# Performance work log

Hardware: AMD Instinct MI355X
Metric: run time of the kernel (lower is better)

Reference implementation:

```python
import jax, jax.numpy as jnp
import numpy as np

HID = 512      # hidden_dim
SEQ = 784      # sequence length hard-coded via make_discrete_HiPPO_nojit(hidden, 784)
BATCH = 1024
OUT = 10


def make_discrete_hippo(N, L):
    # HiPPO-LegS continuous matrices (standard construction)
    n = np.arange(N, dtype=np.float64)
    P = np.sqrt(1.0 + 2.0 * n)
    A = P[:, None] * P[None, :]
    A = -(np.tril(A) - np.diag(n))          # (N, N)
    B = np.sqrt(2.0 * n + 1.0).reshape(N, 1)  # (N, 1)
    # bilinear (Tustin) discretization with step = 1/L
    step = 1.0 / L
    I = np.eye(N)
    BL = np.linalg.inv(I - (step / 2.0) * A)
    Ad = BL @ (I + (step / 2.0) * A)
    Bd = (BL * step) @ B
    return jnp.asarray(Ad, jnp.float32), jnp.asarray(Bd[:, 0], jnp.float32)


def setup_inputs() -> dict:
    key = jax.random.key(0)
    k1, k2, k3, k4 = jax.random.split(key, 4)
    x = jax.random.normal(k1, (BATCH, SEQ), jnp.float32)
    # xavier-uniform C params (flax nn.initializers.xavier_uniform)
    a0 = float(np.sqrt(6.0 / (1 + HID)))
    a1 = float(np.sqrt(6.0 / (HID + HID)))
    C0 = jax.random.uniform(k2, (1, HID), jnp.float32, -a0, a0)
    C1 = jax.random.uniform(k3, (HID, HID), jnp.float32, -a1, a1)
    # final Dense(output_dim): lecun_normal kernel, zero bias
    W = jax.random.normal(k4, (HID, OUT), jnp.float32) / np.sqrt(HID)
    b = jnp.zeros((OUT,), jnp.float32)
    return {"x": x, "C0": C0, "C1": C1, "W": W, "b": b}


def _ssm_layer(A, Bvec, C, u):
    # u: (batch, seq) scalar input per step; returns ys: (seq, batch, d_out)
    def step(h, u_t):  # h: (batch, HID), u_t: (batch,)
        h_next = jnp.tanh(h @ A.T + u_t[:, None] * Bvec[None, :])
        y = h_next @ C.T
        return h_next, y
    h0 = jnp.zeros((u.shape[0], HID), u.dtype)
    _, ys = jax.lax.scan(step, h0, u.T)
    return ys


def reference(x, C0, C1, W, b):
    A, Bvec = make_discrete_hippo(HID, SEQ)  # trace-time constants
    y0 = _ssm_layer(A, Bvec, C0, x)[:, :, 0].T   # (batch, seq) scalar stream
    y1 = _ssm_layer(A, Bvec, C1, y0)             # (seq, batch, HID)
    logits = y1[-1] @ W + b                      # last timestep -> Dense
    return logits
```

## Files before the change

kernel.cpp:

```cpp
#include <hip/hip_runtime.h>
#include <math.h>

#define SEQL 784
#define HIDN 512
#define OUTD 10

typedef float v2 __attribute__((ext_vector_type(2)));

template<int CTRL, int RM>
__device__ __forceinline__ float dpp0(float v) {
    int r = __builtin_amdgcn_update_dpp(0, __builtin_bit_cast(int, v),
                                        CTRL, RM, 0xF, true);
    return __builtin_bit_cast(float, r);
}
__device__ __forceinline__ v2 sp(float v) { v2 r; r.x = v; r.y = v; return r; }
__device__ __forceinline__ v2 vfma(v2 a, v2 b, v2 c) {
    return __builtin_elementwise_fma(a, b, c);
}

__global__ __launch_bounds__(256) void compute_M(const float* __restrict__ C1,
                                                 const float* __restrict__ W,
                                                 float* __restrict__ M) {
    __shared__ float Ws[HIDN * OUTD];
    __shared__ float red[4][64][OUTD];
    const int lane = threadIdx.x & 63, w = threadIdx.x >> 6;
    const int i = blockIdx.x * 64 + lane;
    for (int idx = threadIdx.x; idx < HIDN * OUTD; idx += 256) Ws[idx] = W[idx];
    __syncthreads();
    float acc[OUTD];
#pragma unroll
    for (int o = 0; o < OUTD; ++o) acc[o] = 0.f;
    for (int j = w * 128; j < w * 128 + 128; ++j) {
        float cv = C1[j * HIDN + i];
#pragma unroll
        for (int o = 0; o < OUTD; ++o) acc[o] = fmaf(cv, Ws[j * OUTD + o], acc[o]);
    }
#pragma unroll
    for (int o = 0; o < OUTD; ++o) red[w][lane][o] = acc[o];
    __syncthreads();
    if (w == 0) {
#pragma unroll
        for (int o = 0; o < OUTD; ++o)
            M[i * OUTD + o] = (red[0][lane][o] + red[1][lane][o]) +
                              (red[2][lane][o] + red[3][lane][o]);
    }
}

#define LVL(CTRL, RM, L) {                                                   \
        s.x = fmaf(dpp0<CTRL, RM>(s.x), bc[L], s.x);                         \
        s.x = fmaf(dpp0<CTRL, RM>(r.x), ac[L], s.x);                         \
        s.y = fmaf(dpp0<CTRL, RM>(s.y), bc[L], s.y);                         \
        s.y = fmaf(dpp0<CTRL, RM>(r.y), ac[L], s.y);                         \
        r.x += dpp0<CTRL, RM>(r.x);                                          \
        r.y += dpp0<CTRL, RM>(r.y); }

template<int PSEL>
static __device__ __forceinline__ float do_step(
        v2 (&H)[8], v2 du,
        const float (&P2)[8], const float (&G2)[8], const float (&mE2)[8],
        const float (&K_)[8], const float (&Psp)[8],
        const float (&C0d2)[8], float PiL,
        const float (&ac)[6], const float (&bc)[6]) {
    v2 w8[8];
    v2 rt = sp(-1568.0f) * du;
    v2 in0 = vfma(sp(mE2[0]), rt, H[0]);
    w8[0] = in0;
    v2 sg = sp(Psp[0]) * in0;
    rt = vfma(sp(P2[0]), H[0], rt);
#pragma unroll
    for (int j = 1; j < 8; ++j) {
        v2 in_ = vfma(sp(mE2[j]), rt, H[j]);
        w8[j] = vfma(sp(K_[j]), sg, in_);
        sg = vfma(sp(Psp[j]), in_, sg);
        rt = vfma(sp(P2[j]), H[j], rt);
    }
    v2 r = vfma(sp(1568.0f), du, rt);
    v2 s = sp(PiL) * sg;

    LVL(0x111, 0xF, 0)
    LVL(0x112, 0xF, 1)
    LVL(0x114, 0xF, 2)
    LVL(0x118, 0xF, 3)
    LVL(0x142, 0xA, 4)
    LVL(0x143, 0xC, 5)

    v2 t = r + s, S0;
    S0.x = dpp0<0x138, 0xF>(t.x);  S0.y = dpp0<0x138, 0xF>(t.y);

    v2 yy[8], ep[8];
    float pm[8], rp[8];
#pragma unroll
    for (int j = 0; j < 8; ++j)
        yy[j] = vfma(sp(K_[j]), S0, w8[j]);
#pragma unroll
    for (int j = 0; j < 8; ++j) {
        v2 E;
        E.x = __builtin_amdgcn_exp2f(yy[j].x);
        E.y = __builtin_amdgcn_exp2f(yy[j].y);
        ep[j] = vfma(E, sp(0.5f), sp(0.5f));
    }
#pragma unroll
    for (int j = 0; j < 8; ++j) pm[j] = ep[j].x * ep[j].y;
#pragma unroll
    for (int j = 0; j < 8; ++j) rp[j] = __builtin_amdgcn_rcpf(pm[j]);
    float part = 0.f;
#pragma unroll
    for (int j = 0; j < 8; ++j) {
        float nt = -G2[j] * rp[j];
        v2 hn = vfma(ep[j], sp(nt), sp(G2[j]));
        H[j] = hn;
        part = fmaf(C0d2[j], PSEL ? hn.y : hn.x, part);
    }
    part += dpp0<0x111, 0xF>(part);
    part += dpp0<0x112, 0xF>(part);
    part += dpp0<0x114, 0xF>(part);
    part += dpp0<0x118, 0xF>(part);
    part += dpp0<0x142, 0xA>(part);
    part += dpp0<0x143, 0xC>(part);
    return part;
}

__global__ __launch_bounds__(256, 1) void ssm_main(const float* __restrict__ x,
                                                   const float* __restrict__ C0,
                                                   const float* __restrict__ Mmat,
                                                   const float* __restrict__ bias,
                                                   float* __restrict__ out) {
    const int tid = threadIdx.x;
    const int wave = tid >> 6;
    const int lane = tid & 63;
    const int row = blockIdx.x * 4 + wave;

    __shared__ __align__(16) float xs[4][SEQL + 8];

    const float DEL = 1.0f / 784.0f;
    {
        const float4* __restrict__ xv =
            (const float4*)(x + (size_t)blockIdx.x * 4 * SEQL);
#pragma unroll
        for (int it = 0; it < 4; ++it) {
            int idx = tid + it * 256;
            if (idx < SEQL) {
                float4 v = xv[idx];
                int r = idx / (SEQL / 4);
                int c = (idx % (SEQL / 4)) * 4;
                float4 w;
                w.x = DEL * v.x; w.y = DEL * v.y;
                w.z = DEL * v.z; w.w = DEL * v.w;
                *(float4*)&xs[r][c] = w;
            }
        }
    }
    if (tid < 32) xs[tid >> 3][SEQL + (tid & 7)] = 0.f;
    __syncthreads();

    const double cd = 1.0 / 1568.0;
    const double F = 2.0 * 1.4426950408889634;
    float P2[8], G2[8], mE2[8], C0d2[8], K_[8], Psp[8], PiL;
    double apD = 0.0, bpD = 1.0;
    double Aprod = 1.0;
#pragma unroll
    for (int j = 0; j < 8; ++j) {
        int i = lane * 8 + j;
        double Pd = sqrt(1.0 + 2.0 * (double)i);
        double dd = 1.0 + cd * (double)(i + 1);
        double fd = 1.0 / dd;
        double ad = (1.0 - cd * (double)i) * fd;
        double mEd = -cd * Pd * fd;
        double ed = Pd * mEd;
        double Gd = (1.0 - cd * (double)(i + 1)) * fd;
        double G2d = F * Gd;
        apD = ad * apD + ed;
        bpD = ad * bpD;
        P2[j]  = (float)(Pd / G2d);
        G2[j]  = (float)G2d;
        mE2[j] = (float)(F * mEd);
        K_[j]  = (float)(F * mEd * Aprod);
        Psp[j] = (float)((Pd / F) / (Aprod * ad));
        Aprod *= ad;
        C0d2[j] = (float)((double)DEL * (double)C0[i] / G2d);
    }
    PiL = (float)Aprod;
    float ac[6], bc[6];
    {
        double al = apD, be = bpD;
        int rl = lane & 15;
#pragma unroll
        for (int L = 0; L < 4; ++L) {
            int d = 1 << L;
            ac[L] = (float)al; bc[L] = (float)be;
            double pa = __shfl_up(al, d, 64);
            double pb = __shfl_up(be, d, 64);
            if (rl >= d) { al += be * pa; be *= pb; }
        }
        ac[4] = (float)al; bc[4] = (float)be;
        {
            int src = (lane & 32) + 15;
            double pa = __shfl(al, src, 64);
            double pb = __shfl(be, src, 64);
            if (lane & 16) { al += be * pa; be *= pb; }
        }
        ac[5] = (float)al; bc[5] = (float)be;
        {
            double pa = __shfl(al, 31, 64);
            double pb = __shfl(be, 31, 64);
            if (lane >= 32) { al += be * pa; be *= pb; }
        }
    }

    v2 H[8];
#pragma unroll
    for (int j = 0; j < 8; ++j) H[j] = sp(0.f);

    float y0_d1 = 0.f, y0_d2 = 0.f;
    const float* xrow = xs[wave];

    for (int p = 0; p < 98; ++p) {
        const float4* up = (const float4*)&xrow[p * 8];
        float4 u0 = up[0], u1v = up[1];
        float ub[8] = {u0.x, u0.y, u0.z, u0.w, u1v.x, u1v.y, u1v.z, u1v.w};
#pragma unroll
        for (int q = 0; q < 4; ++q) {
            {
                v2 du; du.x = ub[2 * q]; du.y = y0_d2;
                float part = do_step<1>(H, du, P2, G2, mE2, K_, Psp, C0d2, PiL,
                                        ac, bc);
                y0_d2 = y0_d1;
                y0_d1 = __builtin_bit_cast(float,
                          __builtin_amdgcn_readlane(__builtin_bit_cast(int, part), 63));
            }
            {
                v2 du; du.x = y0_d2; du.y = ub[2 * q + 1];
                float part = do_step<0>(H, du, P2, G2, mE2, K_, Psp, C0d2, PiL,
                                        ac, bc);
                y0_d2 = y0_d1;
                y0_d1 = __builtin_bit_cast(float,
                          __builtin_amdgcn_readlane(__builtin_bit_cast(int, part), 63));
            }
        }
    }
    {
        v2 du; du.x = 0.f; du.y = y0_d2;
        float part = do_step<1>(H, du, P2, G2, mE2, K_, Psp, C0d2, PiL, ac, bc);
        y0_d2 = y0_d1;
        y0_d1 = __builtin_bit_cast(float,
                  __builtin_amdgcn_readlane(__builtin_bit_cast(int, part), 63));
        (void)part;
    }
    {
        v2 du; du.x = y0_d2; du.y = 0.f;
        do_step<0>(H, du, P2, G2, mE2, K_, Psp, C0d2, PiL, ac, bc);
    }

    float acc[OUTD];
#pragma unroll
    for (int o = 0; o < OUTD; ++o) acc[o] = 0.f;
#pragma unroll
    for (int j = 0; j < 8; ++j) {
        float hv = H[j].y / G2[j];
        int i = lane * 8 + j;
#pragma unroll
        for (int o = 0; o < OUTD; ++o)
            acc[o] = fmaf(hv, Mmat[i * OUTD + o], acc[o]);
    }
#pragma unroll
    for (int o = 0; o < OUTD; ++o) {
#pragma unroll
        for (int d = 32; d; d >>= 1) acc[o] += __shfl_xor(acc[o], d, 64);
    }
    if (lane == 0) {
#pragma unroll
        for (int o = 0; o < OUTD; ++o) out[row * OUTD + o] = acc[o] + bias[o];
    }
}

extern "C" void kernel_launch(void* const* d_in, const int* in_sizes, int n_in,
                              void* d_out, int out_size, void* d_ws, size_t ws_size,
                              hipStream_t stream) {
    const float* x  = (const float*)d_in[0];
    const float* C0 = (const float*)d_in[1];
    const float* C1 = (const float*)d_in[2];
    const float* W  = (const float*)d_in[3];
    const float* b  = (const float*)d_in[4];
    float* M = (float*)d_ws;

    compute_M<<<dim3(8), dim3(256), 0, stream>>>(C1, W, M);
    ssm_main<<<dim3(256), dim3(256), 0, stream>>>(x, C0, M, b, (float*)d_out);
}
```

Before: 376.1 us.

## Rotate step boundary so tanh epilogue fuses with next step's prefix scan input

Restructures the per-step loop so each step begins with the exp/rcp nonlinearity of the previous step's pre-activations and immediately feeds each resulting H[j] into the triangular prefix computation. The output reduction is now issued before the DPP scan, so the y0 readlane comes at the end of the same step and the two-step delay line is replaced by a single carried value. The intent is to interleave transcendental and FMA work and shorten the serial dependency chain per timestep. The final hidden state is recomputed after the loop from the carried pre-activations, which changes the timestep at which y0 feedback is consumed and needs checking for equivalence.

```diff
diff --git a/kernel.cpp b/kernel.cpp
--- a/kernel.cpp
+++ b/kernel.cpp
@@ -54,28 +54,44 @@
         r.x += dpp0<CTRL, RM>(r.x);                                          \
         r.y += dpp0<CTRL, RM>(r.y); }
 
-template<int PSEL>
-static __device__ __forceinline__ float do_step(
-        v2 (&H)[8], v2 du,
+template<int PAR>
+static __device__ __forceinline__ void fstep(
+        v2 (&w8)[8], v2& S0, float& y0cur, float u,
         const float (&P2)[8], const float (&G2)[8], const float (&mE2)[8],
         const float (&K_)[8], const float (&Psp)[8],
         const float (&C0d2)[8], float PiL,
         const float (&ac)[6], const float (&bc)[6]) {
-    v2 w8[8];
+    v2 du;
+    if (PAR) { du.x = y0cur; du.y = u; } else { du.x = u; du.y = y0cur; }
     v2 rt = sp(-1568.0f) * du;
-    v2 in0 = vfma(sp(mE2[0]), rt, H[0]);
-    w8[0] = in0;
-    v2 sg = sp(Psp[0]) * in0;
-    rt = vfma(sp(P2[0]), H[0], rt);
-#pragma unroll
-    for (int j = 1; j < 8; ++j) {
-        v2 in_ = vfma(sp(mE2[j]), rt, H[j]);
-        w8[j] = vfma(sp(K_[j]), sg, in_);
-        sg = vfma(sp(Psp[j]), in_, sg);
-        rt = vfma(sp(P2[j]), H[j], rt);
+    v2 sg = sp(0.f);
+    float part = 0.f;
+#pragma unroll
+    for (int j = 0; j < 8; ++j) {
+        v2 yy = vfma(sp(K_[j]), S0, w8[j]);
+        v2 E;
+        E.x = __builtin_amdgcn_exp2f(yy.x);
+        E.y = __builtin_amdgcn_exp2f(yy.y);
+        v2 ep = vfma(E, sp(0.5f), sp(0.5f));
+        float rp = __builtin_amdgcn_rcpf(ep.x * ep.y);
+        float nt = -G2[j] * rp;
+        v2 Hj = vfma(ep, sp(nt), sp(G2[j]));
+        float hl1 = PAR ? Hj.y : Hj.x;
+        part = fmaf(C0d2[j], hl1, part);
+        v2 in_ = vfma(sp(mE2[j]), rt, Hj);
+        w8[j] = (j == 0) ? in_ : vfma(sp(K_[j]), sg, in_);
+        sg = (j == 0) ? sp(Psp[0]) * in_ : vfma(sp(Psp[j]), in_, sg);
+        rt = vfma(sp(P2[j]), Hj, rt);
     }
     v2 r = vfma(sp(1568.0f), du, rt);
     v2 s = sp(PiL) * sg;
+
+    part += dpp0<0x111, 0xF>(part);
+    part += dpp0<0x112, 0xF>(part);
+    part += dpp0<0x114, 0xF>(part);
+    part += dpp0<0x118, 0xF>(part);
+    part += dpp0<0x142, 0xA>(part);
+    part += dpp0<0x143, 0xC>(part);
 
     LVL(0x111, 0xF, 0)
     LVL(0x112, 0xF, 1)
@@ -84,40 +100,11 @@
     LVL(0x142, 0xA, 4)
     LVL(0x143, 0xC, 5)
 
-    v2 t = r + s, S0;
-    S0.x = dpp0<0x138, 0xF>(t.x);  S0.y = dpp0<0x138, 0xF>(t.y);
-
-    v2 yy[8], ep[8];
-    float pm[8], rp[8];
-#pragma unroll
-    for (int j = 0; j < 8; ++j)
-        yy[j] = vfma(sp(K_[j]), S0, w8[j]);
-#pragma unroll
-    for (int j = 0; j < 8; ++j) {
-        v2 E;
-        E.x = __builtin_amdgcn_exp2f(yy[j].x);
-        E.y = __builtin_amdgcn_exp2f(yy[j].y);
-        ep[j] = vfma(E, sp(0.5f), sp(0.5f));
-    }
-#pragma unroll
-    for (int j = 0; j < 8; ++j) pm[j] = ep[j].x * ep[j].y;
-#pragma unroll
-    for (int j = 0; j < 8; ++j) rp[j] = __builtin_amdgcn_rcpf(pm[j]);
-    float part = 0.f;
-#pragma unroll
-    for (int j = 0; j < 8; ++j) {
-        float nt = -G2[j] * rp[j];
-        v2 hn = vfma(ep[j], sp(nt), sp(G2[j]));
-        H[j] = hn;
-        part = fmaf(C0d2[j], PSEL ? hn.y : hn.x, part);
-    }
-    part += dpp0<0x111, 0xF>(part);
-    part += dpp0<0x112, 0xF>(part);
-    part += dpp0<0x114, 0xF>(part);
-    part += dpp0<0x118, 0xF>(part);
-    part += dpp0<0x142, 0xA>(part);
-    part += dpp0<0x143, 0xC>(part);
-    return part;
+    v2 t = r + s;
+    S0.x = dpp0<0x138, 0xF>(t.x);
+    S0.y = dpp0<0x138, 0xF>(t.y);
+    y0cur = __builtin_bit_cast(float,
+              __builtin_amdgcn_readlane(__builtin_bit_cast(int, part), 63));
 }
 
 __global__ __launch_bounds__(256, 1) void ssm_main(const float* __restrict__ x,
@@ -207,11 +194,10 @@
         }
     }
 
-    v2 H[8];
-#pragma unroll
-    for (int j = 0; j < 8; ++j) H[j] = sp(0.f);
-
-    float y0_d1 = 0.f, y0_d2 = 0.f;
+    v2 w8[8], S0 = sp(0.f);
+#pragma unroll
+    for (int j = 0; j < 8; ++j) w8[j] = sp(0.f);
+    float y0cur = 0.f;
     const float* xrow = xs[wave];
 
     for (int p = 0; p < 98; ++p) {
@@ -220,35 +206,25 @@
         float ub[8] = {u0.x, u0.y, u0.z, u0.w, u1v.x, u1v.y, u1v.z, u1v.w};
 #pragma unroll
         for (int q = 0; q < 4; ++q) {
-            {
-                v2 du; du.x = ub[2 * q]; du.y = y0_d2;
-                float part = do_step<1>(H, du, P2, G2, mE2, K_, Psp, C0d2, PiL,
-                                        ac, bc);
-                y0_d2 = y0_d1;
-                y0_d1 = __builtin_bit_cast(float,
-                          __builtin_amdgcn_readlane(__builtin_bit_cast(int, part), 63));
-            }
-            {
-                v2 du; du.x = y0_d2; du.y = ub[2 * q + 1];
-                float part = do_step<0>(H, du, P2, G2, mE2, K_, Psp, C0d2, PiL,
-                                        ac, bc);
-                y0_d2 = y0_d1;
-                y0_d1 = __builtin_bit_cast(float,
-                          __builtin_amdgcn_readlane(__builtin_bit_cast(int, part), 63));
-            }
-        }
-    }
-    {
-        v2 du; du.x = 0.f; du.y = y0_d2;
-        float part = do_step<1>(H, du, P2, G2, mE2, K_, Psp, C0d2, PiL, ac, bc);
-        y0_d2 = y0_d1;
-        y0_d1 = __builtin_bit_cast(float,
-                  __builtin_amdgcn_readlane(__builtin_bit_cast(int, part), 63));
-        (void)part;
-    }
-    {
-        v2 du; du.x = y0_d2; du.y = 0.f;
-        do_step<0>(H, du, P2, G2, mE2, K_, Psp, C0d2, PiL, ac, bc);
+            fstep<0>(w8, S0, y0cur, ub[2 * q],     P2, G2, mE2, K_, Psp,
+                     C0d2, PiL, ac, bc);
+            fstep<1>(w8, S0, y0cur, ub[2 * q + 1], P2, G2, mE2, K_, Psp,
+                     C0d2, PiL, ac, bc);
+        }
+    }
+    fstep<0>(w8, S0, y0cur, 0.f, P2, G2, mE2, K_, Psp, C0d2, PiL, ac, bc);
+    fstep<1>(w8, S0, y0cur, 0.f, P2, G2, mE2, K_, Psp, C0d2, PiL, ac, bc);
+
+    float hv[8];
+#pragma unroll
+    for (int j = 0; j < 8; ++j) {
+        v2 yy = vfma(sp(K_[j]), S0, w8[j]);
+        v2 E;
+        E.x = __builtin_amdgcn_exp2f(yy.x);
+        E.y = __builtin_amdgcn_exp2f(yy.y);
+        v2 ep = vfma(E, sp(0.5f), sp(0.5f));
+        float rp = __builtin_amdgcn_rcpf(ep.x * ep.y);
+        hv[j] = fmaf(-rp, ep.y, 1.0f);
     }
 
     float acc[OUTD];
@@ -256,11 +232,10 @@
     for (int o = 0; o < OUTD; ++o) acc[o] = 0.f;
 #pragma unroll
     for (int j = 0; j < 8; ++j) {
-        float hv = H[j].y / G2[j];
         int i = lane * 8 + j;
 #pragma unroll
         for (int o = 0; o < OUTD; ++o)
-            acc[o] = fmaf(hv, Mmat[i * OUTD + o], acc[o]);
+            acc[o] = fmaf(hv[j], Mmat[i * OUTD + o], acc[o]);
     }
 #pragma unroll
     for (int o = 0; o < OUTD; ++o) {
```

Result: faster. 357.6 us, median of 2 (-4.9%).
